# Optimization experiments

Hardware: AMD Instinct MI355X
Metric: run time of the kernel (lower is better)

The kernel has to match this reference:

```python
import jax, jax.numpy as jnp
import numpy as np

N_NODES, N_EDGES, N_GRAPHS = 50000, 500000, 64
NODE_D, EDGE_D, GLOB_D = 256, 128, 64
EPS = 1e-5


def setup_inputs() -> dict:
    key = jax.random.key(0)
    ks = jax.random.split(key, 12)
    inp = {
        "x": jax.random.normal(ks[0], (N_NODES, NODE_D), jnp.float32),
        "edge_attr": jax.random.normal(ks[1], (N_EDGES, EDGE_D), jnp.float32),
        "u": jax.random.normal(ks[2], (N_GRAPHS, GLOB_D), jnp.float32),
        "W1": jax.random.normal(ks[3], (NODE_D + EDGE_D, 4 * EDGE_D), jnp.float32) * 0.02,
        "b1": jnp.zeros((4 * EDGE_D,), jnp.float32),
        "W2": jax.random.normal(ks[4], (4 * EDGE_D, EDGE_D), jnp.float32) * 0.02,
        "b2": jnp.zeros((EDGE_D,), jnp.float32),
        "W3": jax.random.normal(ks[5], (NODE_D + EDGE_D + GLOB_D, 4 * NODE_D), jnp.float32) * 0.02,
        "b3": jnp.zeros((4 * NODE_D,), jnp.float32),
        "W4": jax.random.normal(ks[6], (4 * NODE_D, NODE_D), jnp.float32) * 0.02,
        "b4": jnp.zeros((NODE_D,), jnp.float32),
        "gamma": jnp.ones((NODE_D,), jnp.float32),
        "beta": jnp.zeros((NODE_D,), jnp.float32),
        "edge_index": jax.random.randint(ks[7], (2, N_EDGES), 0, N_NODES, jnp.int64 if jax.config.jax_enable_x64 else jnp.int32),
        "batch": jnp.sort(jax.random.randint(ks[8], (N_NODES,), 0, N_GRAPHS, jnp.int64 if jax.config.jax_enable_x64 else jnp.int32)),
    }
    return inp


def reference(x, edge_attr, u, W1, b1, W2, b2, W3, b3, W4, b4, gamma, beta, edge_index, batch):
    row, col = edge_index[0], edge_index[1]
    n = x.shape[0]
    # edge MLP on [x[row] || edge_attr]
    e = jnp.concatenate([x[row], edge_attr], axis=1)            # [E, node+edge]
    e = jnp.maximum(e @ W1 + b1, 0.0) @ W2 + b2                 # [E, edge]
    # scatter-mean by destination node
    s = jax.ops.segment_sum(e, col, num_segments=n)             # [N, edge]
    cnt = jax.ops.segment_sum(jnp.ones((col.shape[0],), x.dtype), col, num_segments=n)
    agg = s / jnp.maximum(cnt, 1.0)[:, None]
    # node update MLP on [x || agg || u[batch]]
    h = jnp.concatenate([x, agg, u[batch]], axis=1)             # [N, node+edge+glob]
    h = jnp.maximum(h @ W3 + b3, 0.0) @ W4 + b4                 # [N, node]
    # residual + layernorm (dropout p=0 -> identity)
    y = h + x
    mu = jnp.mean(y, axis=-1, keepdims=True)
    var = jnp.mean((y - mu) ** 2, axis=-1, keepdims=True)
    return (y - mu) * jax.lax.rsqrt(var + EPS) * gamma + beta
```

## Files before the change

kernel.cpp:

```cpp
#include <hip/hip_runtime.h>
#include <stdint.h>

#define NE 500000
#define NN 50000
#define ND 256
#define ED 128
#define GD 64
#define MAXDEG 64

typedef float f4v __attribute__((ext_vector_type(4)));
typedef short s8v __attribute__((ext_vector_type(8)));
typedef short s4v __attribute__((ext_vector_type(4)));

static __device__ __forceinline__ short f2bf(float f) {
  union { float f; uint32_t u; } v; v.f = f;
  uint32_t r = v.u + 0x7FFFu + ((v.u >> 16) & 1u);
  return (short)(r >> 16);
}
static __device__ __forceinline__ float bf2f(uint32_t u) {
  union { uint32_t u; float f; } v; v.u = u << 16; return v.f;
}

static __device__ __forceinline__ void gload_lds16(const void* g, void* l) {
  __builtin_amdgcn_global_load_lds(
      (const __attribute__((address_space(1))) unsigned int*)g,
      (__attribute__((address_space(3))) unsigned int*)l,
      16, 0, 0);
}

static __device__ __forceinline__ void pack_one(const float* __restrict__ src,
                                                short* __restrict__ dst, int C, int idx) {
  int k = idx / C, c = idx - k * C;
  int ks = k >> 5, kh = (k >> 3) & 3, j = k & 7;
  dst[(((ks * C + c) * 4 + kh) << 3) + j] = f2bf(src[idx]);
}

#define J0 3200000
#define J1 196608
#define J2 65536
#define J3 458752
#define J4 262144
#define J5 500000
__global__ void prep_kernel(const float* __restrict__ x, short* __restrict__ xbf,
                            const float* __restrict__ W1, const float* __restrict__ W2,
                            const float* __restrict__ W3, const float* __restrict__ W4,
                            short* __restrict__ w1p, short* __restrict__ w2p,
                            short* __restrict__ w3p, short* __restrict__ w4p,
                            const int* __restrict__ ecol, unsigned int* __restrict__ cnt,
                            int* __restrict__ elist) {
  int idx = blockIdx.x * blockDim.x + threadIdx.x;
  if (idx < J0) {
    int i = idx * 4;
    const float4 v = *(const float4*)(x + i);
    s4v o; o[0] = f2bf(v.x); o[1] = f2bf(v.y); o[2] = f2bf(v.z); o[3] = f2bf(v.w);
    *(s4v*)(xbf + i) = o;
    return;
  }
  idx -= J0;
  if (idx < J1) { pack_one(W1, w1p, 512, idx); return; }
  idx -= J1;
  if (idx < J2) { pack_one(W2, w2p, 128, idx); return; }
  idx -= J2;
  if (idx < J3) { pack_one(W3, w3p, 1024, idx); return; }
  idx -= J3;
  if (idx < J4) { pack_one(W4, w4p, 256, idx); return; }
  idx -= J4;
  if (idx < J5) {
    int c = ecol[idx];
    unsigned int slot = atomicAdd(&cnt[c], 1u);
    if (slot < MAXDEG) elist[c * MAXDEG + slot] = idx;
  }
}

__global__ void agg_kernel(const unsigned short* __restrict__ ebuf,
                           const int* __restrict__ elist,
                           const unsigned int* __restrict__ cnt,
                           unsigned short* __restrict__ aggbf) {
  int tid = threadIdx.x;
  int lane = tid & 63;
  int node = blockIdx.x * 4 + (tid >> 6);
  if (node >= NN) return;
  unsigned int deg = cnt[node];
  unsigned int jend = deg < MAXDEG ? deg : MAXDEG;
  const int jg = lane >> 4;
  const int ch = lane & 15;
  float a[8] = {0.f, 0.f, 0.f, 0.f, 0.f, 0.f, 0.f, 0.f};
  const int* el = elist + (size_t)node * MAXDEG;
  for (unsigned int j = jg; j < jend; j += 4) {
    int eid = el[j];
    s8v v = *(const s8v*)(ebuf + (size_t)eid * ED + ch * 8);
    #pragma unroll
    for (int i = 0; i < 8; ++i) a[i] += bf2f((uint32_t)(uint16_t)v[i]);
  }
  #pragma unroll
  for (int d = 16; d < 64; d <<= 1) {
    #pragma unroll
    for (int i = 0; i < 8; ++i) a[i] += __shfl_xor(a[i], d);
  }
  if (jg == 0) {
    float rc = 1.0f / (deg > 0 ? (float)deg : 1.0f);
    s8v o;
    #pragma unroll
    for (int i = 0; i < 8; ++i) o[i] = f2bf(a[i] * rc);
    *(s8v*)(aggbf + (size_t)node * ED + ch * 8) = o;
  }
}

__launch_bounds__(1024, 4)
__global__ void edge_kernel(const short* __restrict__ xbf,
                            const float* __restrict__ edge_attr,
                            const short* __restrict__ w1p,
                            const float* __restrict__ b1,
                            const short* __restrict__ w2p,
                            const float* __restrict__ b2,
                            const int* __restrict__ erow,
                            unsigned short* __restrict__ ebuf) {
  __shared__ __align__(16) short smem[81920];
  char* const Xb = (char*)smem;
  char* const Eb = (char*)smem + 65536;
  char* const Hb = (char*)smem + 98304;
  const int tid = threadIdx.x;
  const int lane = tid & 63;
  const int w = tid >> 6;
  const int lh = lane >> 4;
  const int ll = lane & 15;
  const int e0 = blockIdx.x * 128;

  {
    #pragma unroll
    for (int i = 0; i < 4; ++i) {
      int p = w * 4 + i;
      int row = 2 * p + (lane >> 5);
      int rid = erow[e0 + row];
      int cg = (lane & 31) ^ (row & 7);
      gload_lds16(xbf + (size_t)rid * 256 + cg * 8, Xb + p * 1024);
    }
  }

  #pragma unroll
  for (int it = 0; it < 2; ++it) {
    int id = tid + it * 1024;
    int row = id >> 4, oct = id & 15;
    s8v vals = {0, 0, 0, 0, 0, 0, 0, 0};
    if (e0 + row < NE) {
      const float* p = edge_attr + (size_t)(e0 + row) * ED + oct * 8;
      const float4 v0 = *(const float4*)(p);
      const float4 v1 = *(const float4*)(p + 4);
      vals[0] = f2bf(v0.x); vals[1] = f2bf(v0.y); vals[2] = f2bf(v0.z); vals[3] = f2bf(v0.w);
      vals[4] = f2bf(v1.x); vals[5] = f2bf(v1.y); vals[6] = f2bf(v1.z); vals[7] = f2bf(v1.w);
    }
    *(s8v*)(Eb + row * 256 + ((oct ^ (row & 7)) << 4)) = vals;
  }
  __syncthreads();

  f4v acc1[2][8];
  #pragma unroll
  for (int n = 0; n < 2; ++n)
    #pragma unroll
    for (int m = 0; m < 8; ++m)
      acc1[n][m] = (f4v){0.f, 0.f, 0.f, 0.f};

  for (int ks = 0; ks < 8; ++ks) {
    s8v wf0 = *(const s8v*)(w1p + (((ks * 512 + w * 16 + ll) * 4 + lh) << 3));
    s8v wf1 = *(const s8v*)(w1p + (((ks * 512 + 256 + w * 16 + ll) * 4 + lh) << 3));
    #pragma unroll
    for (int mh = 0; mh < 2; ++mh) {
      s8v hf[4];
      #pragma unroll
      for (int m = 0; m < 4; ++m) {
        int row = 64 * mh + 16 * m + ll;
        int byte = row * 512 + (((ks * 4 + lh) ^ (row & 7)) << 4);
        hf[m] = *(const s8v*)(Xb + byte);
      }
      #pragma unroll
      for (int m = 0; m < 4; ++m) {
        acc1[0][4 * mh + m] = __builtin_amdgcn_mfma_f32_16x16x32_bf16(wf0, hf[m], acc1[0][4 * mh + m], 0, 0, 0);
        acc1[1][4 * mh + m] = __builtin_amdgcn_mfma_f32_16x16x32_bf16(wf1, hf[m], acc1[1][4 * mh + m], 0, 0, 0);
      }
    }
  }
  for (int ks = 8; ks < 12; ++ks) {
    s8v wf0 = *(const s8v*)(w1p + (((ks * 512 + w * 16 + ll) * 4 + lh) << 3));
    s8v wf1 = *(const s8v*)(w1p + (((ks * 512 + 256 + w * 16 + ll) * 4 + lh) << 3));
    #pragma unroll
    for (int mh = 0; mh < 2; ++mh) {
      s8v hf[4];
      #pragma unroll
      for (int m = 0; m < 4; ++m) {
        int row = 64 * mh + 16 * m + ll;
        int byte = row * 256 + ((((ks - 8) * 4 + lh) ^ (row & 7)) << 4);
        hf[m] = *(const s8v*)(Eb + byte);
      }
      #pragma unroll
      for (int m = 0; m < 4; ++m) {
        acc1[0][4 * mh + m] = __builtin_amdgcn_mfma_f32_16x16x32_bf16(wf0, hf[m], acc1[0][4 * mh + m], 0, 0, 0);
        acc1[1][4 * mh + m] = __builtin_amdgcn_mfma_f32_16x16x32_bf16(wf1, hf[m], acc1[1][4 * mh + m], 0, 0, 0);
      }
    }
  }

  {
    int lcb = w * 16 + 4 * lh;
    const float4 bv = *(const float4*)(b1 + lcb);
    #pragma unroll
    for (int m = 0; m < 8; ++m) {
      int row = 16 * m + ll;
      s4v o;
      float v0 = acc1[0][m][0] + bv.x; o[0] = f2bf(v0 > 0.f ? v0 : 0.f);
      float v1 = acc1[0][m][1] + bv.y; o[1] = f2bf(v1 > 0.f ? v1 : 0.f);
      float v2 = acc1[0][m][2] + bv.z; o[2] = f2bf(v2 > 0.f ? v2 : 0.f);
      float v3 = acc1[0][m][3] + bv.w; o[3] = f2bf(v3 > 0.f ? v3 : 0.f);
      int byte = (row * 512 + lcb * 2) ^ ((row & 7) << 4);
      *(s4v*)(Hb + byte) = o;
    }
  }
  __syncthreads();

  {
    int lcb = w * 16 + 4 * lh;
    const float4 bv = *(const float4*)(b1 + 256 + lcb);
    #pragma unroll
    for (int m = 0; m < 8; ++m) {
      int row = 16 * m + ll;
      s4v o;
      float v0 = acc1[1][m][0] + bv.x; o[0] = f2bf(v0 > 0.f ? v0 : 0.f);
      float v1 = acc1[1][m][1] + bv.y; o[1] = f2bf(v1 > 0.f ? v1 : 0.f);
      float v2 = acc1[1][m][2] + bv.z; o[2] = f2bf(v2 > 0.f ? v2 : 0.f);
      float v3 = acc1[1][m][3] + bv.w; o[3] = f2bf(v3 > 0.f ? v3 : 0.f);
      int byte = (row * 512 + lcb * 2) ^ ((row & 7) << 4);
      *(s4v*)(Xb + byte) = o;
    }
  }
  __syncthreads();

  f4v acc2[4];
  #pragma unroll
  for (int m = 0; m < 4; ++m)
    acc2[m] = (f4v){0.f, 0.f, 0.f, 0.f};

  for (int ks = 0; ks < 8; ++ks) {
    s8v wf = *(const s8v*)(w2p + (((ks * 128 + (w & 7) * 16 + ll) * 4 + lh) << 3));
    #pragma unroll
    for (int m = 0; m < 4; ++m) {
      int row = 64 * (w >> 3) + 16 * m + ll;
      int byte = (row * 512 + ks * 64 + lh * 16) ^ ((row & 7) << 4);
      s8v hf = *(const s8v*)(Hb + byte);
      acc2[m] = __builtin_amdgcn_mfma_f32_16x16x32_bf16(wf, hf, acc2[m], 0, 0, 0);
    }
  }
  for (int ks = 8; ks < 16; ++ks) {
    s8v wf = *(const s8v*)(w2p + (((ks * 128 + (w & 7) * 16 + ll) * 4 + lh) << 3));
    #pragma unroll
    for (int m = 0; m < 4; ++m) {
      int row = 64 * (w >> 3) + 16 * m + ll;
      int byte = (row * 512 + (ks - 8) * 64 + lh * 16) ^ ((row & 7) << 4);
      s8v hf = *(const s8v*)(Xb + byte);
      acc2[m] = __builtin_amdgcn_mfma_f32_16x16x32_bf16(wf, hf, acc2[m], 0, 0, 0);
    }
  }

  {
    int cb = (w & 7) * 16 + 4 * lh;
    const float4 bv = *(const float4*)(b2 + cb);
    #pragma unroll
    for (int m = 0; m < 4; ++m) {
      int row = 64 * (w >> 3) + 16 * m + ll;
      int e = e0 + row;
      if (e < NE) {
        s4v o;
        o[0] = f2bf(acc2[m][0] + bv.x);
        o[1] = f2bf(acc2[m][1] + bv.y);
        o[2] = f2bf(acc2[m][2] + bv.z);
        o[3] = f2bf(acc2[m][3] + bv.w);
        *(s4v*)(ebuf + (size_t)e * ED + cb) = o;
      }
    }
  }
}

__launch_bounds__(1024, 4)
__global__ void node_kernel(const float* __restrict__ x,
                            const short* __restrict__ xbf,
                            const float* __restrict__ u,
                            const short* __restrict__ w3p,
                            const float* __restrict__ b3,
                            const short* __restrict__ w4p,
                            const float* __restrict__ b4,
                            const float* __restrict__ gamma,
                            const float* __restrict__ beta,
                            const int* __restrict__ batch,
                            const unsigned short* __restrict__ aggbf,
                            float* __restrict__ out) {
  __shared__ __align__(16) short smem[64 * 1024];
  const int tid = threadIdx.x;
  const int lane = tid & 63;
  const int w = tid >> 6;
  const int lh = lane >> 4;
  const int ll = lane & 15;
  const int n0 = blockIdx.x * 64;

  #pragma unroll
  for (int it = 0; it < 4; ++it) {
    int ch = tid + it * 1024;
    if (ch < 3584) {
      int rr = ch / 56;
      int cc = (ch - rr * 56) * 8;
      s8v vals = {0, 0, 0, 0, 0, 0, 0, 0};
      int node = n0 + rr;
      if (node < NN) {
        if (cc < 256) {
          vals = *(const s8v*)(xbf + (size_t)node * ND + cc);
        } else if (cc < 384) {
          vals = *(const s8v*)(aggbf + (size_t)node * ED + (cc - 256));
        } else {
          const float* up = u + (size_t)batch[node] * GD + (cc - 384);
          const float4 v0 = *(const float4*)(up);
          const float4 v1 = *(const float4*)(up + 4);
          vals[0] = f2bf(v0.x); vals[1] = f2bf(v0.y); vals[2] = f2bf(v0.z); vals[3] = f2bf(v0.w);
          vals[4] = f2bf(v1.x); vals[5] = f2bf(v1.y); vals[6] = f2bf(v1.z); vals[7] = f2bf(v1.w);
        }
      }
      int byte = (rr * 896 + cc * 2) ^ ((rr & 7) << 4);
      *(s8v*)((char*)smem + byte) = vals;
    }
  }
  __syncthreads();

  f4v acc3[4][4];
  #pragma unroll
  for (int n = 0; n < 4; ++n)
    #pragma unroll
    for (int m = 0; m < 4; ++m)
      acc3[n][m] = (f4v){0.f, 0.f, 0.f, 0.f};

  for (int ks = 0; ks < 14; ++ks) {
    s8v af[4];
    #pragma unroll
    for (int m = 0; m < 4; ++m) {
      int row = 16 * m + ll;
      int byte = (row * 896 + ks * 64 + lh * 16) ^ ((row & 7) << 4);
      af[m] = *(const s8v*)((const char*)smem + byte);
    }
    #pragma unroll
    for (int n = 0; n < 4; ++n) {
      s8v wf = *(const s8v*)(w3p + (((ks * 1024 + w * 64 + 16 * n + ll) * 4 + lh) << 3));
      #pragma unroll
      for (int m = 0; m < 4; ++m)
        acc3[n][m] = __builtin_amdgcn_mfma_f32_16x16x32_bf16(wf, af[m], acc3[n][m], 0, 0, 0);
    }
  }
  __syncthreads();

  #pragma unroll
  for (int n = 0; n < 4; ++n) {
    int cb = w * 64 + 16 * n + 4 * lh;
    const float4 bv = *(const float4*)(b3 + cb);
    #pragma unroll
    for (int m = 0; m < 4; ++m) {
      int row = 16 * m + ll;
      s4v o;
      float v0 = acc3[n][m][0] + bv.x; o[0] = f2bf(v0 > 0.f ? v0 : 0.f);
      float v1 = acc3[n][m][1] + bv.y; o[1] = f2bf(v1 > 0.f ? v1 : 0.f);
      float v2 = acc3[n][m][2] + bv.z; o[2] = f2bf(v2 > 0.f ? v2 : 0.f);
      float v3 = acc3[n][m][3] + bv.w; o[3] = f2bf(v3 > 0.f ? v3 : 0.f);
      int byte = (row * 2048 + cb * 2) ^ ((row & 7) << 4);
      *(s4v*)((char*)smem + byte) = o;
    }
  }
  __syncthreads();

  f4v acc4[4];
  #pragma unroll
  for (int m = 0; m < 4; ++m)
    acc4[m] = (f4v){0.f, 0.f, 0.f, 0.f};

  for (int ks = 0; ks < 32; ++ks) {
    s8v wf = *(const s8v*)(w4p + (((ks * 256 + w * 16 + ll) * 4 + lh) << 3));
    #pragma unroll
    for (int m = 0; m < 4; ++m) {
      int row = 16 * m + ll;
      int byte = (row * 2048 + ks * 64 + lh * 16) ^ ((row & 7) << 4);
      s8v hf = *(const s8v*)((const char*)smem + byte);
      acc4[m] = __builtin_amdgcn_mfma_f32_16x16x32_bf16(wf, hf, acc4[m], 0, 0, 0);
    }
  }
  __syncthreads();

  float* yb = (float*)smem;
  {
    int cb = w * 16 + 4 * lh;
    const float4 bv = *(const float4*)(b4 + cb);
    #pragma unroll
    for (int m = 0; m < 4; ++m) {
      int row = 16 * m + ll;
      int node = n0 + row;
      float4 xv = {0.f, 0.f, 0.f, 0.f};
      if (node < NN) xv = *(const float4*)(x + (size_t)node * ND + cb);
      f4v o;
      o[0] = acc4[m][0] + bv.x + xv.x;
      o[1] = acc4[m][1] + bv.y + xv.y;
      o[2] = acc4[m][2] + bv.z + xv.z;
      o[3] = acc4[m][3] + bv.w + xv.w;
      *(f4v*)(yb + row * 260 + cb) = o;
    }
  }
  __syncthreads();

  {
    int row = tid >> 4, sub = tid & 15;
    int node = n0 + row;
    float v[16];
    float sum = 0.f, ssq = 0.f;
    #pragma unroll
    for (int i = 0; i < 4; ++i) {
      const float4 t = *(const float4*)(yb + row * 260 + (i * 16 + sub) * 4);
      v[i * 4 + 0] = t.x; v[i * 4 + 1] = t.y; v[i * 4 + 2] = t.z; v[i * 4 + 3] = t.w;
      sum += t.x + t.y + t.z + t.w;
      ssq += t.x * t.x + t.y * t.y + t.z * t.z + t.w * t.w;
    }
    #pragma unroll
    for (int d = 1; d < 16; d <<= 1) {
      sum += __shfl_xor(sum, d);
      ssq += __shfl_xor(ssq, d);
    }
    float mu = sum * (1.f / 256.f);
    float var = ssq * (1.f / 256.f) - mu * mu;
    float rstd = rsqrtf(var + 1e-5f);
    if (node < NN) {
      #pragma unroll
      for (int i = 0; i < 4; ++i) {
        int c = (i * 16 + sub) * 4;
        const float4 g = *(const float4*)(gamma + c);
        const float4 be = *(const float4*)(beta + c);
        float4 o;
        o.x = (v[i * 4 + 0] - mu) * rstd * g.x + be.x;
        o.y = (v[i * 4 + 1] - mu) * rstd * g.y + be.y;
        o.z = (v[i * 4 + 2] - mu) * rstd * g.z + be.z;
        o.w = (v[i * 4 + 3] - mu) * rstd * g.w + be.w;
        *(float4*)(out + (size_t)node * ND + c) = o;
      }
    }
  }
}

extern "C" void kernel_launch(void* const* d_in, const int* in_sizes, int n_in,
                              void* d_out, int out_size, void* d_ws, size_t ws_size,
                              hipStream_t stream) {
  const float* x    = (const float*)d_in[0];
  const float* ea   = (const float*)d_in[1];
  const float* u    = (const float*)d_in[2];
  const float* W1   = (const float*)d_in[3];
  const float* b1   = (const float*)d_in[4];
  const float* W2   = (const float*)d_in[5];
  const float* b2   = (const float*)d_in[6];
  const float* W3   = (const float*)d_in[7];
  const float* b3   = (const float*)d_in[8];
  const float* W4   = (const float*)d_in[9];
  const float* b4   = (const float*)d_in[10];
  const float* gamma = (const float*)d_in[11];
  const float* beta  = (const float*)d_in[12];
  const int* eidx   = (const int*)d_in[13];
  const int* batch  = (const int*)d_in[14];
  float* out = (float*)d_out;

  char* p = (char*)d_ws;
  size_t off = 0;
  auto take = [&](size_t n) { char* r = p + off; off = (off + n + 255) & ~(size_t)255; return r; };
  short* xbf = (short*)take((size_t)NN * ND * 2);
  short* w1p = (short*)take((size_t)384 * 512 * 2);
  short* w2p = (short*)take((size_t)512 * 128 * 2);
  short* w3p = (short*)take((size_t)448 * 1024 * 2);
  short* w4p = (short*)take((size_t)1024 * 256 * 2);
  unsigned int* cnt = (unsigned int*)take((size_t)NN * 4);
  int* elist = (int*)take((size_t)NN * MAXDEG * 4);
  unsigned short* aggbf = (unsigned short*)take((size_t)NN * ED * 2);
  unsigned short* ebuf = (unsigned short*)take((size_t)NE * ED * 2);

  const int* erow = eidx;
  const int* ecol = eidx + NE;

  hipMemsetAsync(cnt, 0, (size_t)NN * 4, stream);
  {
    const int total = J0 + J1 + J2 + J3 + J4 + J5;
    prep_kernel<<<(total + 255) / 256, 256, 0, stream>>>(x, xbf, W1, W2, W3, W4,
                                                         w1p, w2p, w3p, w4p,
                                                         ecol, cnt, elist);
  }
  edge_kernel<<<(NE + 127) / 128, 1024, 0, stream>>>(xbf, ea, w1p, b1, w2p, b2, erow, ebuf);
  agg_kernel<<<(NN + 3) / 4, 256, 0, stream>>>(ebuf, elist, cnt, aggbf);
  node_kernel<<<(NN + 63) / 64, 1024, 0, stream>>>(x, xbf, u, w3p, b3, w4p, b4,
                                                   gamma, beta, batch, aggbf, out);
}
```

Baseline: 649.4 us.

## Split node-kernel LDS staging into per-part regions and halve hidden-buffer barrier

The node kernel now stages x, agg and u into separate swizzled LDS regions, loading x directly into LDS with global_load_lds instead of going through registers. The first half of the hidden activations goes to a region that does not overlap the inputs, so waves 0-7 can write it without waiting on a barrier. The second GEMM is split into two K halves with a barrier between them. The prep kernel also moves the edge-bucketing atomics to the front of its index range so that work is issued first. The aim is to remove barrier stalls and staging overhead, in exchange for more complex indexing and a different block ordering in prep.

```diff
diff --git a/kernel.cpp b/kernel.cpp
--- a/kernel.cpp
+++ b/kernel.cpp
@@ -35,12 +35,12 @@
   dst[(((ks * C + c) * 4 + kh) << 3) + j] = f2bf(src[idx]);
 }
 
+#define J5 500000
 #define J0 3200000
 #define J1 196608
 #define J2 65536
 #define J3 458752
 #define J4 262144
-#define J5 500000
 __global__ void prep_kernel(const float* __restrict__ x, short* __restrict__ xbf,
                             const float* __restrict__ W1, const float* __restrict__ W2,
                             const float* __restrict__ W3, const float* __restrict__ W4,
@@ -49,6 +49,13 @@
                             const int* __restrict__ ecol, unsigned int* __restrict__ cnt,
                             int* __restrict__ elist) {
   int idx = blockIdx.x * blockDim.x + threadIdx.x;
+  if (idx < J5) {
+    int c = ecol[idx];
+    unsigned int slot = atomicAdd(&cnt[c], 1u);
+    if (slot < MAXDEG) elist[c * MAXDEG + slot] = idx;
+    return;
+  }
+  idx -= J5;
   if (idx < J0) {
     int i = idx * 4;
     const float4 v = *(const float4*)(x + i);
@@ -64,12 +71,6 @@
   if (idx < J3) { pack_one(W3, w3p, 1024, idx); return; }
   idx -= J3;
   if (idx < J4) { pack_one(W4, w4p, 256, idx); return; }
-  idx -= J4;
-  if (idx < J5) {
-    int c = ecol[idx];
-    unsigned int slot = atomicAdd(&cnt[c], 1u);
-    if (slot < MAXDEG) elist[c * MAXDEG + slot] = idx;
-  }
 }
 
 __global__ void agg_kernel(const unsigned short* __restrict__ ebuf,
@@ -291,7 +292,12 @@
                             const int* __restrict__ batch,
                             const unsigned short* __restrict__ aggbf,
                             float* __restrict__ out) {
-  __shared__ __align__(16) short smem[64 * 1024];
+  __shared__ __align__(16) short smem[65536];
+  char* const Xn = (char*)smem;
+  char* const An = (char*)smem + 32768;
+  char* const Un = (char*)smem + 49152;
+  char* const H1r = (char*)smem;
+  char* const H0r = (char*)smem + 65536;
   const int tid = threadIdx.x;
   const int lane = tid & 63;
   const int w = tid >> 6;
@@ -299,30 +305,35 @@
   const int ll = lane & 15;
   const int n0 = blockIdx.x * 64;
 
-  #pragma unroll
-  for (int it = 0; it < 4; ++it) {
-    int ch = tid + it * 1024;
-    if (ch < 3584) {
-      int rr = ch / 56;
-      int cc = (ch - rr * 56) * 8;
-      s8v vals = {0, 0, 0, 0, 0, 0, 0, 0};
-      int node = n0 + rr;
-      if (node < NN) {
-        if (cc < 256) {
-          vals = *(const s8v*)(xbf + (size_t)node * ND + cc);
-        } else if (cc < 384) {
-          vals = *(const s8v*)(aggbf + (size_t)node * ED + (cc - 256));
-        } else {
-          const float* up = u + (size_t)batch[node] * GD + (cc - 384);
-          const float4 v0 = *(const float4*)(up);
-          const float4 v1 = *(const float4*)(up + 4);
-          vals[0] = f2bf(v0.x); vals[1] = f2bf(v0.y); vals[2] = f2bf(v0.z); vals[3] = f2bf(v0.w);
-          vals[4] = f2bf(v1.x); vals[5] = f2bf(v1.y); vals[6] = f2bf(v1.z); vals[7] = f2bf(v1.w);
-        }
-      }
-      int byte = (rr * 896 + cc * 2) ^ ((rr & 7) << 4);
-      *(s8v*)((char*)smem + byte) = vals;
-    }
+  {
+    #pragma unroll
+    for (int i = 0; i < 2; ++i) {
+      int p = w * 2 + i;
+      int row = 2 * p + (lane >> 5);
+      int node = n0 + row; if (node >= NN) node = NN - 1;
+      int cg = (lane & 31) ^ (row & 7);
+      gload_lds16(xbf + (size_t)node * 256 + cg * 8, Xn + p * 1024);
+    }
+  }
+  {
+    int row = tid >> 4, oct = tid & 15;
+    s8v v = {0, 0, 0, 0, 0, 0, 0, 0};
+    int node = n0 + row;
+    if (node < NN) v = *(const s8v*)(aggbf + (size_t)node * ED + oct * 8);
+    *(s8v*)(An + row * 256 + ((oct ^ (row & 7)) << 4)) = v;
+  }
+  if (tid < 512) {
+    int row = tid >> 3, oct = tid & 7;
+    s8v v = {0, 0, 0, 0, 0, 0, 0, 0};
+    int node = n0 + row;
+    if (node < NN) {
+      const float* up = u + (size_t)batch[node] * GD + oct * 8;
+      const float4 v0 = *(const float4*)(up);
+      const float4 v1 = *(const float4*)(up + 4);
+      v[0] = f2bf(v0.x); v[1] = f2bf(v0.y); v[2] = f2bf(v0.z); v[3] = f2bf(v0.w);
+      v[4] = f2bf(v1.x); v[5] = f2bf(v1.y); v[6] = f2bf(v1.z); v[7] = f2bf(v1.w);
+    }
+    *(s8v*)(Un + row * 128 + ((oct ^ (row & 7)) << 4)) = v;
   }
   __syncthreads();
 
@@ -338,8 +349,12 @@
     #pragma unroll
     for (int m = 0; m < 4; ++m) {
       int row = 16 * m + ll;
-      int byte = (row * 896 + ks * 64 + lh * 16) ^ ((row & 7) << 4);
-      af[m] = *(const s8v*)((const char*)smem + byte);
+      int byte;
+      if (ks < 8)       byte = row * 512 + (((ks * 4 + lh) ^ (row & 7)) << 4);
+      else if (ks < 12) byte = row * 256 + ((((ks - 8) * 4 + lh) ^ (row & 7)) << 4);
+      else              byte = row * 128 + ((((ks - 12) * 4 + lh) ^ (row & 7)) << 4);
+      const char* base = (ks < 8) ? Xn : (ks < 12) ? An : Un;
+      af[m] = *(const s8v*)(base + byte);
     }
     #pragma unroll
     for (int n = 0; n < 4; ++n) {
@@ -349,38 +364,70 @@
         acc3[n][m] = __builtin_amdgcn_mfma_f32_16x16x32_bf16(wf, af[m], acc3[n][m], 0, 0, 0);
     }
   }
-  __syncthreads();
-
-  #pragma unroll
-  for (int n = 0; n < 4; ++n) {
-    int cb = w * 64 + 16 * n + 4 * lh;
-    const float4 bv = *(const float4*)(b3 + cb);
-    #pragma unroll
-    for (int m = 0; m < 4; ++m) {
-      int row = 16 * m + ll;
-      s4v o;
-      float v0 = acc3[n][m][0] + bv.x; o[0] = f2bf(v0 > 0.f ? v0 : 0.f);
-      float v1 = acc3[n][m][1] + bv.y; o[1] = f2bf(v1 > 0.f ? v1 : 0.f);
-      float v2 = acc3[n][m][2] + bv.z; o[2] = f2bf(v2 > 0.f ? v2 : 0.f);
-      float v3 = acc3[n][m][3] + bv.w; o[3] = f2bf(v3 > 0.f ? v3 : 0.f);
-      int byte = (row * 2048 + cb * 2) ^ ((row & 7) << 4);
-      *(s4v*)((char*)smem + byte) = o;
-    }
-  }
-  __syncthreads();
+
+  if (w < 8) {
+    #pragma unroll
+    for (int n = 0; n < 4; ++n) {
+      int lc = w * 64 + 16 * n + 4 * lh;
+      const float4 bv = *(const float4*)(b3 + lc);
+      #pragma unroll
+      for (int m = 0; m < 4; ++m) {
+        int row = 16 * m + ll;
+        s4v o;
+        float v0 = acc3[n][m][0] + bv.x; o[0] = f2bf(v0 > 0.f ? v0 : 0.f);
+        float v1 = acc3[n][m][1] + bv.y; o[1] = f2bf(v1 > 0.f ? v1 : 0.f);
+        float v2 = acc3[n][m][2] + bv.z; o[2] = f2bf(v2 > 0.f ? v2 : 0.f);
+        float v3 = acc3[n][m][3] + bv.w; o[3] = f2bf(v3 > 0.f ? v3 : 0.f);
+        int byte = (row * 1024 + lc * 2) ^ ((row & 7) << 4);
+        *(s4v*)(H0r + byte) = o;
+      }
+    }
+  }
+  __syncthreads();
+
+  if (w >= 8) {
+    #pragma unroll
+    for (int n = 0; n < 4; ++n) {
+      int lc = (w - 8) * 64 + 16 * n + 4 * lh;
+      const float4 bv = *(const float4*)(b3 + 512 + lc);
+      #pragma unroll
+      for (int m = 0; m < 4; ++m) {
+        int row = 16 * m + ll;
+        s4v o;
+        float v0 = acc3[n][m][0] + bv.x; o[0] = f2bf(v0 > 0.f ? v0 : 0.f);
+        float v1 = acc3[n][m][1] + bv.y; o[1] = f2bf(v1 > 0.f ? v1 : 0.f);
+        float v2 = acc3[n][m][2] + bv.z; o[2] = f2bf(v2 > 0.f ? v2 : 0.f);
+        float v3 = acc3[n][m][3] + bv.w; o[3] = f2bf(v3 > 0.f ? v3 : 0.f);
+        int byte = (row * 1024 + lc * 2) ^ ((row & 7) << 4);
+        *(s4v*)(H1r + byte) = o;
+      }
+    }
+  }
 
   f4v acc4[4];
   #pragma unroll
   for (int m = 0; m < 4; ++m)
     acc4[m] = (f4v){0.f, 0.f, 0.f, 0.f};
 
-  for (int ks = 0; ks < 32; ++ks) {
+  for (int ks = 0; ks < 16; ++ks) {
     s8v wf = *(const s8v*)(w4p + (((ks * 256 + w * 16 + ll) * 4 + lh) << 3));
     #pragma unroll
     for (int m = 0; m < 4; ++m) {
       int row = 16 * m + ll;
-      int byte = (row * 2048 + ks * 64 + lh * 16) ^ ((row & 7) << 4);
-      s8v hf = *(const s8v*)((const char*)smem + byte);
+      int byte = (row * 1024 + ks * 64 + lh * 16) ^ ((row & 7) << 4);
+      s8v hf = *(const s8v*)(H0r + byte);
+      acc4[m] = __builtin_amdgcn_mfma_f32_16x16x32_bf16(wf, hf, acc4[m], 0, 0, 0);
+    }
+  }
+  __syncthreads();
+
+  for (int ks = 16; ks < 32; ++ks) {
+    s8v wf = *(const s8v*)(w4p + (((ks * 256 + w * 16 + ll) * 4 + lh) << 3));
+    #pragma unroll
+    for (int m = 0; m < 4; ++m) {
+      int row = 16 * m + ll;
+      int byte = (row * 1024 + (ks - 16) * 64 + lh * 16) ^ ((row & 7) << 4);
+      s8v hf = *(const s8v*)(H1r + byte);
       acc4[m] = __builtin_amdgcn_mfma_f32_16x16x32_bf16(wf, hf, acc4[m], 0, 0, 0);
     }
   }
@@ -481,7 +528,7 @@
 
   hipMemsetAsync(cnt, 0, (size_t)NN * 4, stream);
   {
-    const int total = J0 + J1 + J2 + J3 + J4 + J5;
+    const int total = J5 + J0 + J1 + J2 + J3 + J4;
     prep_kernel<<<(total + 255) / 256, 256, 0, stream>>>(x, xbf, W1, W2, W3, W4,
                                                          w1p, w2p, w3p, w4p,
                                                          ecol, cnt, elist);
```

After: 584.2 us (median of 2 runs). 10.0% less time.
